# Optimization experiments

Hardware: AMD Instinct MI355X
Metric: run time of the kernel (lower is better)

The kernel has to match this reference:

```python
import jax, jax.numpy as jnp
import numpy as np


def setup_inputs() -> dict:
    key = jax.random.key(0)
    k1, k2 = jax.random.split(key)
    B, R1, R2, D = 16, 2048, 2048, 256
    matrix_1 = jax.random.normal(k1, (B, R1, D), dtype=jnp.float32)
    matrix_2 = jax.random.normal(k2, (B, R2, D), dtype=jnp.float32)
    return {"matrix_1": matrix_1, "matrix_2": matrix_2}


def reference(matrix_1, matrix_2):
    # Original keras layer tiles matrix_1 to [B, R1, R2, D] and matrix_2 to
    # [B, R1, R2, D], then applies the dot-product similarity (elementwise
    # multiply + sum over last dim). That is exactly a batched matmul:
    #   scores[b, i, j] = sum_d matrix_1[b, i, d] * matrix_2[b, j, d]
    return jnp.einsum('bid,bjd->bij', matrix_1, matrix_2)
```

## Files before the change

### kernel.cpp

```cpp
#include <hip/hip_runtime.h>
#include <hip/hip_bf16.h>
#include <stdint.h>


typedef _Float16 f16x8 __attribute__((ext_vector_type(8)));
typedef _Float16 f16x4 __attribute__((ext_vector_type(4)));
typedef _Float16 f16x2 __attribute__((ext_vector_type(2)));
typedef float f32x4 __attribute__((ext_vector_type(4)));

#define NB 16
#define DM 2048
#define DN 2048
#define DK 256
#define BM 128
#define BN 128
#define BK 32
#define BKP 36
#define NT (DK / BK)
#define NWG (NB * (DM/BM) * (DN/BN))

#define LDS_BARRIER() do {                                   \
    asm volatile("s_waitcnt lgkmcnt(0)" ::: "memory");       \
    __builtin_amdgcn_s_barrier();                            \
    asm volatile("" ::: "memory");                           \
} while (0)

__global__ __launch_bounds__(256, 2) void fused_gemm(const float* __restrict__ A,
                                                     const float* __restrict__ B,
                                                     float* __restrict__ C) {
    __shared__ _Float16 As[2][BM * BKP];
    __shared__ _Float16 Bs[2][BN * BKP];

    const int t = threadIdx.x;

    const int bid = blockIdx.x;
    const int swz = (bid & 7) * (NWG / 8) + (bid >> 3);
    const int b    = swz >> 8;
    const int rem  = swz & 255;
    const int brow = (rem >> 4) << 7;
    const int bcol = (rem & 15) << 7;

    const float* At = A + (size_t)b * DM * DK + (size_t)brow * DK;
    const float* Bt = B + (size_t)b * DN * DK + (size_t)bcol * DK;

    const int w    = t >> 6;
    const int l    = t & 63;
    const int wr   = (w >> 1) * 64;
    const int wc   = (w & 1) * 64;
    const int lrow = l & 15;
    const int lko  = (l >> 4) * 8;

    f32x4 acc[4][4] = {};

    auto issue = [&](int kt, float4 (&va)[4], float4 (&vb)[4]) {
#pragma unroll
        for (int i = 0; i < 4; ++i) {
            const int c = t + i * 256;
            const int r = c >> 3, q = c & 7;
            va[i] = *reinterpret_cast<const float4*>(At + (size_t)r * DK + kt * BK + q * 4);
            vb[i] = *reinterpret_cast<const float4*>(Bt + (size_t)r * DK + kt * BK + q * 4);
        }
    };
    auto wlds = [&](int buf, const float4 (&va)[4], const float4 (&vb)[4]) {
#pragma unroll
        for (int i = 0; i < 4; ++i) {
            const int c = t + i * 256;
            const int r = c >> 3, q = c & 7;
            f16x2 alo = __builtin_bit_cast(f16x2, __builtin_amdgcn_cvt_pkrtz(va[i].x, va[i].y));
            f16x2 ahi = __builtin_bit_cast(f16x2, __builtin_amdgcn_cvt_pkrtz(va[i].z, va[i].w));
            f16x2 blo = __builtin_bit_cast(f16x2, __builtin_amdgcn_cvt_pkrtz(vb[i].x, vb[i].y));
            f16x2 bhi = __builtin_bit_cast(f16x2, __builtin_amdgcn_cvt_pkrtz(vb[i].z, vb[i].w));
            f16x4 ha = { alo[0], alo[1], ahi[0], ahi[1] };
            f16x4 hb = { blo[0], blo[1], bhi[0], bhi[1] };
            *reinterpret_cast<f16x4*>(&As[buf][r * BKP + q * 4]) = ha;
            *reinterpret_cast<f16x4*>(&Bs[buf][r * BKP + q * 4]) = hb;
        }
    };
    auto compute = [&](int buf) {
        f16x8 af[4], bfr[4];
#pragma unroll
        for (int m = 0; m < 4; ++m)
            af[m] = *reinterpret_cast<const f16x8*>(&As[buf][(wr + m * 16 + lrow) * BKP + lko]);
#pragma unroll
        for (int n = 0; n < 4; ++n)
            bfr[n] = *reinterpret_cast<const f16x8*>(&Bs[buf][(wc + n * 16 + lrow) * BKP + lko]);
#pragma unroll
        for (int m = 0; m < 4; ++m)
#pragma unroll
            for (int n = 0; n < 4; ++n)
                acc[m][n] = __builtin_amdgcn_mfma_f32_16x16x32_f16(af[m], bfr[n], acc[m][n], 0, 0, 0);
    };

    float4 vaX[4], vbX[4], vaY[4], vbY[4];

    issue(0, vaX, vbX);
    issue(1, vaY, vbY);
    wlds(0, vaX, vbX);
    LDS_BARRIER();

#pragma unroll
    for (int k2 = 0; k2 < NT; k2 += 2) {
        if (k2 + 2 < NT) issue(k2 + 2, vaX, vbX);
        compute(0);
        wlds(1, vaY, vbY);
        LDS_BARRIER();

        if (k2 + 3 < NT) issue(k2 + 3, vaY, vbY);
        compute(1);
        if (k2 + 2 < NT) {
            wlds(0, vaX, vbX);
        }
        LDS_BARRIER();
    }

    float* Cb = C + (size_t)b * DM * DN;
    const int crow = brow + wr + (l >> 4) * 4;
    const int ccol = bcol + wc + lrow;
#pragma unroll
    for (int m = 0; m < 4; ++m)
#pragma unroll
        for (int j = 0; j < 4; ++j) {
            float* rowp = Cb + (size_t)(crow + m * 16 + j) * DN + ccol;
#pragma unroll
            for (int n = 0; n < 4; ++n)
                __builtin_nontemporal_store(acc[m][n][j], rowp + n * 16);
        }
}

extern "C" void kernel_launch(void* const* d_in, const int* in_sizes, int n_in,
                              void* d_out, int out_size, void* d_ws, size_t ws_size,
                              hipStream_t stream) {
    const float* m1 = (const float*)d_in[0];
    const float* m2 = (const float*)d_in[1];
    float* out = (float*)d_out;
    (void)d_ws; (void)ws_size;

    fused_gemm<<<NWG, 256, 0, stream>>>(m1, m2, out);
}
```

Measured before the change: 75.78 us.

## Split tile into two row phases to overlap first-half stores with second-half loads

Each workgroup now computes its 128x128 output tile as two 64-row phases with separate accumulators. The first half's results are stored while the second phase's global loads are in flight, so epilogue write traffic overlaps with main-loop work. In exchange, the B tile is reloaded and reconverted for each phase, and LDS reads and MFMA operations per barrier are halved, which lowers arithmetic intensity.

```diff
diff --git a/kernel.cpp b/kernel.cpp
--- a/kernel.cpp
+++ b/kernel.cpp
@@ -28,7 +28,7 @@
 __global__ __launch_bounds__(256, 2) void fused_gemm(const float* __restrict__ A,
                                                      const float* __restrict__ B,
                                                      float* __restrict__ C) {
-    __shared__ _Float16 As[2][BM * BKP];
+    __shared__ _Float16 As[2][64 * BKP];
     __shared__ _Float16 Bs[2][BN * BKP];
 
     const int t = threadIdx.x;
@@ -45,86 +45,121 @@
 
     const int w    = t >> 6;
     const int l    = t & 63;
-    const int wr   = (w >> 1) * 64;
+    const int wrp  = (w >> 1) * 32;
     const int wc   = (w & 1) * 64;
     const int lrow = l & 15;
     const int lko  = (l >> 4) * 8;
 
-    f32x4 acc[4][4] = {};
+    f32x4 acc0[2][4] = {};
+    f32x4 acc1[2][4] = {};
+    asm volatile("" :: "v"(acc1[0][0]), "v"(acc1[0][1]), "v"(acc1[0][2]), "v"(acc1[0][3]),
+                       "v"(acc1[1][0]), "v"(acc1[1][1]), "v"(acc1[1][2]), "v"(acc1[1][3]));
 
-    auto issue = [&](int kt, float4 (&va)[4], float4 (&vb)[4]) {
+    auto issueA = [&](int p, int kt, float4 (&ax)[2]) {
+#pragma unroll
+        for (int i = 0; i < 2; ++i) {
+            const int c = t + i * 256;
+            const int r = c >> 3, q = c & 7;
+            ax[i] = *reinterpret_cast<const float4*>(At + (size_t)(p * 64 + r) * DK + kt * BK + q * 4);
+        }
+    };
+    auto issueB = [&](int kt, float4 (&bx)[4]) {
 #pragma unroll
         for (int i = 0; i < 4; ++i) {
             const int c = t + i * 256;
             const int r = c >> 3, q = c & 7;
-            va[i] = *reinterpret_cast<const float4*>(At + (size_t)r * DK + kt * BK + q * 4);
-            vb[i] = *reinterpret_cast<const float4*>(Bt + (size_t)r * DK + kt * BK + q * 4);
+            bx[i] = *reinterpret_cast<const float4*>(Bt + (size_t)r * DK + kt * BK + q * 4);
         }
     };
-    auto wlds = [&](int buf, const float4 (&va)[4], const float4 (&vb)[4]) {
+    auto cvt4 = [](const float4& v) -> f16x4 {
+        f16x2 lo = __builtin_bit_cast(f16x2, __builtin_amdgcn_cvt_pkrtz(v.x, v.y));
+        f16x2 hi = __builtin_bit_cast(f16x2, __builtin_amdgcn_cvt_pkrtz(v.z, v.w));
+        return f16x4{ lo[0], lo[1], hi[0], hi[1] };
+    };
+    auto wldsA = [&](int buf, const float4 (&ax)[2]) {
+#pragma unroll
+        for (int i = 0; i < 2; ++i) {
+            const int c = t + i * 256;
+            const int r = c >> 3, q = c & 7;
+            *reinterpret_cast<f16x4*>(&As[buf][r * BKP + q * 4]) = cvt4(ax[i]);
+        }
+    };
+    auto wldsB = [&](int buf, const float4 (&bx)[4]) {
 #pragma unroll
         for (int i = 0; i < 4; ++i) {
             const int c = t + i * 256;
             const int r = c >> 3, q = c & 7;
-            f16x2 alo = __builtin_bit_cast(f16x2, __builtin_amdgcn_cvt_pkrtz(va[i].x, va[i].y));
-            f16x2 ahi = __builtin_bit_cast(f16x2, __builtin_amdgcn_cvt_pkrtz(va[i].z, va[i].w));
-            f16x2 blo = __builtin_bit_cast(f16x2, __builtin_amdgcn_cvt_pkrtz(vb[i].x, vb[i].y));
-            f16x2 bhi = __builtin_bit_cast(f16x2, __builtin_amdgcn_cvt_pkrtz(vb[i].z, vb[i].w));
-            f16x4 ha = { alo[0], alo[1], ahi[0], ahi[1] };
-            f16x4 hb = { blo[0], blo[1], bhi[0], bhi[1] };
-            *reinterpret_cast<f16x4*>(&As[buf][r * BKP + q * 4]) = ha;
-            *reinterpret_cast<f16x4*>(&Bs[buf][r * BKP + q * 4]) = hb;
+            *reinterpret_cast<f16x4*>(&Bs[buf][r * BKP + q * 4]) = cvt4(bx[i]);
         }
     };
-    auto compute = [&](int buf) {
-        f16x8 af[4], bfr[4];
+    auto compute = [&](int buf, f32x4 (&acc)[2][4]) {
+        f16x8 af[2], bf[4];
 #pragma unroll
-        for (int m = 0; m < 4; ++m)
-            af[m] = *reinterpret_cast<const f16x8*>(&As[buf][(wr + m * 16 + lrow) * BKP + lko]);
+        for (int m = 0; m < 2; ++m)
+            af[m] = *reinterpret_cast<const f16x8*>(&As[buf][(wrp + m * 16 + lrow) * BKP + lko]);
 #pragma unroll
         for (int n = 0; n < 4; ++n)
-            bfr[n] = *reinterpret_cast<const f16x8*>(&Bs[buf][(wc + n * 16 + lrow) * BKP + lko]);
+            bf[n] = *reinterpret_cast<const f16x8*>(&Bs[buf][(wc + n * 16 + lrow) * BKP + lko]);
 #pragma unroll
-        for (int m = 0; m < 4; ++m)
+        for (int m = 0; m < 2; ++m)
 #pragma unroll
             for (int n = 0; n < 4; ++n)
-                acc[m][n] = __builtin_amdgcn_mfma_f32_16x16x32_f16(af[m], bfr[n], acc[m][n], 0, 0, 0);
+                acc[m][n] = __builtin_amdgcn_mfma_f32_16x16x32_f16(af[m], bf[n], acc[m][n], 0, 0, 0);
     };
 
-    float4 vaX[4], vbX[4], vaY[4], vbY[4];
+    float* Cb = C + (size_t)b * DM * DN;
+    auto store_phase = [&](int p, const f32x4 (&acc)[2][4]) {
+        const int crow = brow + p * 64 + wrp + (l >> 4) * 4;
+        const int ccol = bcol + wc + lrow;
+#pragma unroll
+        for (int m = 0; m < 2; ++m)
+#pragma unroll
+            for (int j = 0; j < 4; ++j) {
+                float* rowp = Cb + (size_t)(crow + m * 16 + j) * DN + ccol;
+#pragma unroll
+                for (int n = 0; n < 4; ++n)
+                    __builtin_nontemporal_store(acc[m][n][j], rowp + n * 16);
+            }
+    };
 
-    issue(0, vaX, vbX);
-    issue(1, vaY, vbY);
-    wlds(0, vaX, vbX);
+    float4 axX[2], bxX[4], axY[2], bxY[4];
+
+    issueA(0, 0, axX); issueB(0, bxX);
+    issueA(0, 1, axY); issueB(1, bxY);
+    wldsA(0, axX); wldsB(0, bxX);
+    LDS_BARRIER();
+#pragma unroll
+    for (int k2 = 0; k2 < NT; k2 += 2) {
+        if (k2 + 2 < NT) { issueA(0, k2 + 2, axX); issueB(k2 + 2, bxX); }
+        compute(0, acc0);
+        wldsA(1, axY); wldsB(1, bxY);
+        LDS_BARRIER();
+        if (k2 + 3 < NT) { issueA(0, k2 + 3, axY); issueB(k2 + 3, bxY); }
+        compute(1, acc0);
+        if (k2 + 2 < NT) { wldsA(0, axX); wldsB(0, bxX); }
+        LDS_BARRIER();
+    }
+
+    issueA(1, 0, axX); issueB(0, bxX);
+    issueA(1, 1, axY); issueB(1, bxY);
+    asm volatile("" ::: "memory");
+    store_phase(0, acc0);
+    wldsA(0, axX); wldsB(0, bxX);
     LDS_BARRIER();
 
 #pragma unroll
     for (int k2 = 0; k2 < NT; k2 += 2) {
-        if (k2 + 2 < NT) issue(k2 + 2, vaX, vbX);
-        compute(0);
-        wlds(1, vaY, vbY);
+        if (k2 + 2 < NT) { issueA(1, k2 + 2, axX); issueB(k2 + 2, bxX); }
+        compute(0, acc1);
+        wldsA(1, axY); wldsB(1, bxY);
         LDS_BARRIER();
-
-        if (k2 + 3 < NT) issue(k2 + 3, vaY, vbY);
-        compute(1);
-        if (k2 + 2 < NT) {
-            wlds(0, vaX, vbX);
-        }
+        if (k2 + 3 < NT) { issueA(1, k2 + 3, axY); issueB(k2 + 3, bxY); }
+        compute(1, acc1);
+        if (k2 + 2 < NT) { wldsA(0, axX); wldsB(0, bxX); }
         LDS_BARRIER();
     }
 
-    float* Cb = C + (size_t)b * DM * DN;
-    const int crow = brow + wr + (l >> 4) * 4;
-    const int ccol = bcol + wc + lrow;
-#pragma unroll
-    for (int m = 0; m < 4; ++m)
-#pragma unroll
-        for (int j = 0; j < 4; ++j) {
-            float* rowp = Cb + (size_t)(crow + m * 16 + j) * DN + ccol;
-#pragma unroll
-            for (int n = 0; n < 4; ++n)
-                __builtin_nontemporal_store(acc[m][n][j], rowp + n * 16);
-        }
+    store_phase(1, acc1);
 }
 
 extern "C" void kernel_launch(void* const* d_in, const int* in_sizes, int n_in,
```

Result: slower. 90.88 us (+19.9%).

## Use 512-thread blocks with 8 waves and a single-buffered global prefetch

Applied to the files above, without the earlier changes.

Raises the workgroup from 256 to 512 threads (8 waves, each computing a 32x64 sub-tile instead of 64x64). This halves the accumulator and prefetch registers per thread and raises the launch bound to 4 blocks per CU. The two-deep register prefetch of global tiles becomes a single-stage prefetch, and the last barrier is skipped. In exchange each wave reuses fewer A fragments per B fragment, so LDS read traffic per MFMA goes up, and global latency hiding rests more on occupancy than on prefetch depth.

```diff
diff --git a/kernel.cpp b/kernel.cpp
--- a/kernel.cpp
+++ b/kernel.cpp
@@ -25,7 +25,7 @@
     asm volatile("" ::: "memory");                           \
 } while (0)
 
-__global__ __launch_bounds__(256, 2) void fused_gemm(const float* __restrict__ A,
+__global__ __launch_bounds__(512, 4) void fused_gemm(const float* __restrict__ A,
                                                      const float* __restrict__ B,
                                                      float* __restrict__ C) {
     __shared__ _Float16 As[2][BM * BKP];
@@ -45,79 +45,70 @@
 
     const int w    = t >> 6;
     const int l    = t & 63;
-    const int wr   = (w >> 1) * 64;
-    const int wc   = (w & 1) * 64;
+    const int wrow = (w >> 1) * 32;
+    const int wcol = (w & 1) * 64;
     const int lrow = l & 15;
     const int lko  = (l >> 4) * 8;
 
-    f32x4 acc[4][4] = {};
+    f32x4 acc[2][4] = {};
 
-    auto issue = [&](int kt, float4 (&va)[4], float4 (&vb)[4]) {
+    auto issue = [&](int kt, float4 (&va)[2], float4 (&vb)[2]) {
 #pragma unroll
-        for (int i = 0; i < 4; ++i) {
-            const int c = t + i * 256;
+        for (int i = 0; i < 2; ++i) {
+            const int c = t + i * 512;
             const int r = c >> 3, q = c & 7;
             va[i] = *reinterpret_cast<const float4*>(At + (size_t)r * DK + kt * BK + q * 4);
             vb[i] = *reinterpret_cast<const float4*>(Bt + (size_t)r * DK + kt * BK + q * 4);
         }
     };
-    auto wlds = [&](int buf, const float4 (&va)[4], const float4 (&vb)[4]) {
+    auto cvt4 = [](const float4& v) -> f16x4 {
+        f16x2 lo = __builtin_bit_cast(f16x2, __builtin_amdgcn_cvt_pkrtz(v.x, v.y));
+        f16x2 hi = __builtin_bit_cast(f16x2, __builtin_amdgcn_cvt_pkrtz(v.z, v.w));
+        return f16x4{ lo[0], lo[1], hi[0], hi[1] };
+    };
+    auto wlds = [&](int buf, const float4 (&va)[2], const float4 (&vb)[2]) {
 #pragma unroll
-        for (int i = 0; i < 4; ++i) {
-            const int c = t + i * 256;
+        for (int i = 0; i < 2; ++i) {
+            const int c = t + i * 512;
             const int r = c >> 3, q = c & 7;
-            f16x2 alo = __builtin_bit_cast(f16x2, __builtin_amdgcn_cvt_pkrtz(va[i].x, va[i].y));
-            f16x2 ahi = __builtin_bit_cast(f16x2, __builtin_amdgcn_cvt_pkrtz(va[i].z, va[i].w));
-            f16x2 blo = __builtin_bit_cast(f16x2, __builtin_amdgcn_cvt_pkrtz(vb[i].x, vb[i].y));
-            f16x2 bhi = __builtin_bit_cast(f16x2, __builtin_amdgcn_cvt_pkrtz(vb[i].z, vb[i].w));
-            f16x4 ha = { alo[0], alo[1], ahi[0], ahi[1] };
-            f16x4 hb = { blo[0], blo[1], bhi[0], bhi[1] };
-            *reinterpret_cast<f16x4*>(&As[buf][r * BKP + q * 4]) = ha;
-            *reinterpret_cast<f16x4*>(&Bs[buf][r * BKP + q * 4]) = hb;
+            *reinterpret_cast<f16x4*>(&As[buf][r * BKP + q * 4]) = cvt4(va[i]);
+            *reinterpret_cast<f16x4*>(&Bs[buf][r * BKP + q * 4]) = cvt4(vb[i]);
         }
     };
     auto compute = [&](int buf) {
-        f16x8 af[4], bfr[4];
+        f16x8 af[2], bf[4];
 #pragma unroll
-        for (int m = 0; m < 4; ++m)
-            af[m] = *reinterpret_cast<const f16x8*>(&As[buf][(wr + m * 16 + lrow) * BKP + lko]);
+        for (int m = 0; m < 2; ++m)
+            af[m] = *reinterpret_cast<const f16x8*>(&As[buf][(wrow + m * 16 + lrow) * BKP + lko]);
 #pragma unroll
         for (int n = 0; n < 4; ++n)
-            bfr[n] = *reinterpret_cast<const f16x8*>(&Bs[buf][(wc + n * 16 + lrow) * BKP + lko]);
+            bf[n] = *reinterpret_cast<const f16x8*>(&Bs[buf][(wcol + n * 16 + lrow) * BKP + lko]);
 #pragma unroll
-        for (int m = 0; m < 4; ++m)
+        for (int m = 0; m < 2; ++m)
 #pragma unroll
             for (int n = 0; n < 4; ++n)
-                acc[m][n] = __builtin_amdgcn_mfma_f32_16x16x32_f16(af[m], bfr[n], acc[m][n], 0, 0, 0);
+                acc[m][n] = __builtin_amdgcn_mfma_f32_16x16x32_f16(af[m], bf[n], acc[m][n], 0, 0, 0);
     };
 
-    float4 vaX[4], vbX[4], vaY[4], vbY[4];
+    float4 va[2], vb[2];
 
-    issue(0, vaX, vbX);
-    issue(1, vaY, vbY);
-    wlds(0, vaX, vbX);
+    issue(0, va, vb);
+    wlds(0, va, vb);
     LDS_BARRIER();
 
 #pragma unroll
-    for (int k2 = 0; k2 < NT; k2 += 2) {
-        if (k2 + 2 < NT) issue(k2 + 2, vaX, vbX);
-        compute(0);
-        wlds(1, vaY, vbY);
-        LDS_BARRIER();
-
-        if (k2 + 3 < NT) issue(k2 + 3, vaY, vbY);
-        compute(1);
-        if (k2 + 2 < NT) {
-            wlds(0, vaX, vbX);
-        }
-        LDS_BARRIER();
+    for (int kt = 0; kt < NT; ++kt) {
+        if (kt + 1 < NT) issue(kt + 1, va, vb);
+        compute(kt & 1);
+        if (kt + 1 < NT) wlds((kt + 1) & 1, va, vb);
+        if (kt + 1 < NT) LDS_BARRIER();
     }
 
     float* Cb = C + (size_t)b * DM * DN;
-    const int crow = brow + wr + (l >> 4) * 4;
-    const int ccol = bcol + wc + lrow;
+    const int crow = brow + wrow + (l >> 4) * 4;
+    const int ccol = bcol + wcol + lrow;
 #pragma unroll
-    for (int m = 0; m < 4; ++m)
+    for (int m = 0; m < 2; ++m)
 #pragma unroll
         for (int j = 0; j < 4; ++j) {
             float* rowp = Cb + (size_t)(crow + m * 16 + j) * DN + ccol;
@@ -135,5 +126,5 @@
     float* out = (float*)d_out;
     (void)d_ws; (void)ws_size;
 
-    fused_gemm<<<NWG, 256, 0, stream>>>(m1, m2, out);
+    fused_gemm<<<NWG, 512, 0, stream>>>(m1, m2, out);
 }
```

Result: slower. 96.18 us (+26.9%).

## Process two adjacent column tiles per workgroup and overlap first tile's store

Applied to the files above, without the earlier changes.

Each workgroup now computes a 128x256 output region as two sequential 128x128 tiles, reusing the same A rows, and halves the grid to 2048 workgroups. The first tile's accumulators are written out while the second tile's K-loop proceeds, so store latency overlaps with loads and MFMA work, and workgroup launch overhead is amortized. It doubles accumulator registers (two 4x4 f32x4 sets), which may reduce occupancy or cause spills under launch_bounds(256,2). A is still reloaded from global memory for the second tile rather than kept resident.

```diff
diff --git a/kernel.cpp b/kernel.cpp
--- a/kernel.cpp
+++ b/kernel.cpp
@@ -17,7 +17,8 @@
 #define BK 32
 #define BKP 36
 #define NT (DK / BK)
-#define NWG (NB * (DM/BM) * (DN/BN))
+#define TSTEPS (2 * NT)
+#define NWG 2048
 
 #define LDS_BARRIER() do {                                   \
     asm volatile("s_waitcnt lgkmcnt(0)" ::: "memory");       \
@@ -35,13 +36,13 @@
 
     const int bid = blockIdx.x;
     const int swz = (bid & 7) * (NWG / 8) + (bid >> 3);
-    const int b    = swz >> 8;
-    const int rem  = swz & 255;
-    const int brow = (rem >> 4) << 7;
-    const int bcol = (rem & 15) << 7;
+    const int b    = swz >> 7;
+    const int rem  = swz & 127;
+    const int brow = (rem >> 3) << 7;
+    const int bcol = (rem & 7) << 8;
 
-    const float* At = A + (size_t)b * DM * DK + (size_t)brow * DK;
-    const float* Bt = B + (size_t)b * DN * DK + (size_t)bcol * DK;
+    const float* At  = A + (size_t)b * DM * DK + (size_t)brow * DK;
+    const float* Bt0 = B + (size_t)b * DN * DK + (size_t)bcol * DK;
 
     const int w    = t >> 6;
     const int l    = t & 63;
@@ -50,45 +51,62 @@
     const int lrow = l & 15;
     const int lko  = (l >> 4) * 8;
 
-    f32x4 acc[4][4] = {};
+    f32x4 acc0[4][4] = {};
+    f32x4 acc1[4][4] = {};
 
-    auto issue = [&](int kt, float4 (&va)[4], float4 (&vb)[4]) {
+    auto issue = [&](int s, float4 (&va)[4], float4 (&vb)[4]) {
+        const float* Ap = At + (size_t)(s & 7) * BK;
+        const float* Bp = Bt0 + (size_t)(s >> 3) * BN * DK + (size_t)(s & 7) * BK;
 #pragma unroll
         for (int i = 0; i < 4; ++i) {
             const int c = t + i * 256;
             const int r = c >> 3, q = c & 7;
-            va[i] = *reinterpret_cast<const float4*>(At + (size_t)r * DK + kt * BK + q * 4);
-            vb[i] = *reinterpret_cast<const float4*>(Bt + (size_t)r * DK + kt * BK + q * 4);
+            va[i] = *reinterpret_cast<const float4*>(Ap + (size_t)r * DK + q * 4);
+            vb[i] = *reinterpret_cast<const float4*>(Bp + (size_t)r * DK + q * 4);
         }
+    };
+    auto cvt4 = [](const float4& v) -> f16x4 {
+        f16x2 lo = __builtin_bit_cast(f16x2, __builtin_amdgcn_cvt_pkrtz(v.x, v.y));
+        f16x2 hi = __builtin_bit_cast(f16x2, __builtin_amdgcn_cvt_pkrtz(v.z, v.w));
+        return f16x4{ lo[0], lo[1], hi[0], hi[1] };
     };
     auto wlds = [&](int buf, const float4 (&va)[4], const float4 (&vb)[4]) {
 #pragma unroll
         for (int i = 0; i < 4; ++i) {
             const int c = t + i * 256;
             const int r = c >> 3, q = c & 7;
-            f16x2 alo = __builtin_bit_cast(f16x2, __builtin_amdgcn_cvt_pkrtz(va[i].x, va[i].y));
-            f16x2 ahi = __builtin_bit_cast(f16x2, __builtin_amdgcn_cvt_pkrtz(va[i].z, va[i].w));
-            f16x2 blo = __builtin_bit_cast(f16x2, __builtin_amdgcn_cvt_pkrtz(vb[i].x, vb[i].y));
-            f16x2 bhi = __builtin_bit_cast(f16x2, __builtin_amdgcn_cvt_pkrtz(vb[i].z, vb[i].w));
-            f16x4 ha = { alo[0], alo[1], ahi[0], ahi[1] };
-            f16x4 hb = { blo[0], blo[1], bhi[0], bhi[1] };
-            *reinterpret_cast<f16x4*>(&As[buf][r * BKP + q * 4]) = ha;
-            *reinterpret_cast<f16x4*>(&Bs[buf][r * BKP + q * 4]) = hb;
+            *reinterpret_cast<f16x4*>(&As[buf][r * BKP + q * 4]) = cvt4(va[i]);
+            *reinterpret_cast<f16x4*>(&Bs[buf][r * BKP + q * 4]) = cvt4(vb[i]);
         }
     };
-    auto compute = [&](int buf) {
-        f16x8 af[4], bfr[4];
+    auto compute = [&](int buf, f32x4 (&acc)[4][4]) {
+        f16x8 af[4], bf[4];
 #pragma unroll
         for (int m = 0; m < 4; ++m)
             af[m] = *reinterpret_cast<const f16x8*>(&As[buf][(wr + m * 16 + lrow) * BKP + lko]);
 #pragma unroll
         for (int n = 0; n < 4; ++n)
-            bfr[n] = *reinterpret_cast<const f16x8*>(&Bs[buf][(wc + n * 16 + lrow) * BKP + lko]);
+            bf[n] = *reinterpret_cast<const f16x8*>(&Bs[buf][(wc + n * 16 + lrow) * BKP + lko]);
 #pragma unroll
         for (int m = 0; m < 4; ++m)
 #pragma unroll
             for (int n = 0; n < 4; ++n)
-                acc[m][n] = __builtin_amdgcn_mfma_f32_16x16x32_f16(af[m], bfr[n], acc[m][n], 0, 0, 0);
+                acc[m][n] = __builtin_amdgcn_mfma_f32_16x16x32_f16(af[m], bf[n], acc[m][n], 0, 0, 0);
+    };
+
+    float* Cb = C + (size_t)b * DM * DN;
+    const int crow = brow + wr + (l >> 4) * 4;
+    auto store_tile = [&](int tile, const f32x4 (&acc)[4][4]) {
+        const int ccol = bcol + tile * BN + wc + lrow;
+#pragma unroll
+        for (int m = 0; m < 4; ++m)
+#pragma unroll
+            for (int j = 0; j < 4; ++j) {
+                float* rowp = Cb + (size_t)(crow + m * 16 + j) * DN + ccol;
+#pragma unroll
+                for (int n = 0; n < 4; ++n)
+                    __builtin_nontemporal_store(acc[m][n][j], rowp + n * 16);
+            }
     };
 
     float4 vaX[4], vbX[4], vaY[4], vbY[4];
@@ -99,32 +117,24 @@
     LDS_BARRIER();
 
 #pragma unroll
-    for (int k2 = 0; k2 < NT; k2 += 2) {
-        if (k2 + 2 < NT) issue(k2 + 2, vaX, vbX);
-        compute(0);
+    for (int s2 = 0; s2 < TSTEPS; s2 += 2) {
+        if (s2 + 2 < TSTEPS) issue(s2 + 2, vaX, vbX);
+        if (s2 < NT) compute(0, acc0); else compute(0, acc1);
         wlds(1, vaY, vbY);
         LDS_BARRIER();
 
-        if (k2 + 3 < NT) issue(k2 + 3, vaY, vbY);
-        compute(1);
-        if (k2 + 2 < NT) {
-            wlds(0, vaX, vbX);
+        if (s2 + 3 < TSTEPS) issue(s2 + 3, vaY, vbY);
+        if (s2 + 1 < NT) compute(1, acc0); else compute(1, acc1);
+
+        if (s2 + 1 == NT - 1) {
+            store_tile(0, acc0);
         }
+
+        if (s2 + 2 < TSTEPS) wlds(0, vaX, vbX);
         LDS_BARRIER();
     }
 
-    float* Cb = C + (size_t)b * DM * DN;
-    const int crow = brow + wr + (l >> 4) * 4;
-    const int ccol = bcol + wc + lrow;
-#pragma unroll
-    for (int m = 0; m < 4; ++m)
-#pragma unroll
-        for (int j = 0; j < 4; ++j) {
-            float* rowp = Cb + (size_t)(crow + m * 16 + j) * DN + ccol;
-#pragma unroll
-            for (int n = 0; n < 4; ++n)
-                __builtin_nontemporal_store(acc[m][n][j], rowp + n * 16);
-        }
+    store_tile(1, acc1);
 }
 
 extern "C" void kernel_launch(void* const* d_in, const int* in_sizes, int n_in,
```

After: 83.56 us. 10.3% more time.
